# Kernel optimization log

Hardware: AMD Instinct MI355X
Metric: run time of the kernel (lower is better)

The kernel has to match this reference:

```python
import jax, jax.numpy as jnp
import numpy as np

jax.config.update("jax_enable_x64", True)

N_USERS = 100000
N_ITEMS = 50000
N = N_USERS + N_ITEMS          # total nodes
E = 4_000_000                  # nnz of adj
MASK_DEPTH = 2
KEEP_RATE = 0.1
N_SEEDS = 500


def setup_inputs() -> dict:
    key = jax.random.key(0)
    k1, k2, k3, k4 = jax.random.split(key, 4)
    rows = jax.random.randint(k1, (E,), 0, N, dtype=jnp.int64)
    cols = jax.random.randint(k2, (E,), 0, N, dtype=jnp.int64)
    seeds = jax.random.randint(k3, (N_SEEDS,), 0, N, dtype=jnp.int64)
    adj_vals = jax.random.uniform(k4, (E,), dtype=jnp.float32)
    return {"adj_vals": adj_vals, "rows": rows, "cols": cols, "seeds": seeds}


def _mask_subgraphs(adj_vals, rows, cols, seeds, key):
    # --- vectorized BFS-style edge masking (equivalent to the serial per-seed
    # loop: the set of removed edges per depth is the union over the frontier,
    # and collected endpoints are identical to the sequential version) ---
    alive = jnp.ones(E, dtype=bool)                    # edges not yet masked
    frontier = jnp.zeros(N, dtype=bool).at[seeds].set(True)
    masked_nodes = frontier                            # maskNodes accumulator
    for i in range(MASK_DEPTH):
        idct = (frontier[rows] | frontier[cols]) & alive
        alive = alive & ~idct
        if i != MASK_DEPTH - 1:
            hits = (jnp.zeros(N, jnp.int32)
                    .at[rows].add(idct.astype(jnp.int32))
                    .at[cols].add(idct.astype(jnp.int32)))
            frontier = hits > 0                        # unique(concat(nxtSeeds))
            masked_nodes = masked_nodes | frontier
    # random augmentation of the masked node set
    samp_num = int(N * KEEP_RATE)
    ks, kr, kc = jax.random.split(key, 3)
    sampled = jax.random.randint(ks, (samp_num,), 0, N)
    masked_nodes = masked_nodes.at[sampled].set(True)

    # --- encoderAdj: remaining edges with value 1, symmetric degree norm ---
    alive_f = alive.astype(jnp.float32)
    deg = jnp.zeros(N, jnp.float32).at[rows].add(alive_f)   # sparse row sum
    dnorm = jnp.power(deg + 1e-12, -0.5)
    enc_vals = alive_f * dnorm[rows] * dnorm[cols]          # 0 for masked edges

    # --- decoderAdj: random edges among masked nodes + self loops + remaining
    # edges, dedup'd through the row*N+col hash ---
    order = jnp.argsort(~masked_nodes)        # masked node ids first, ascending
    tem_num = masked_nodes.sum()
    i1 = jnp.minimum((jax.random.uniform(kr, (E,)) * tem_num).astype(jnp.int64),
                     tem_num - 1)
    i2 = jnp.minimum((jax.random.uniform(kc, (E,)) * tem_num).astype(jnp.int64),
                     tem_num - 1)
    tr = order[i1]
    tc = order[i2]
    ar = jnp.arange(N, dtype=jnp.int64)
    # masked (dead) edges collapse onto the (0,0) self-loop hash so the
    # fixed-size unique removes them, mirroring the compaction in torch
    h_tail = jnp.where(alive, rows * N + cols, 0)
    hashv = jnp.concatenate([tr * N + tc, tc * N + tr, ar * (N + 1), h_tail])
    uniq = jnp.unique(hashv, size=hashv.shape[0], fill_value=-1)
    valid = uniq >= 0
    dec_vals = valid.astype(jnp.float32)
    dec_cols = jnp.where(valid, uniq % N, 0)
    dec_rows = jnp.where(valid, uniq // N, 0)
    return rows, cols, enc_vals, dec_rows, dec_cols, dec_vals


def reference(adj_vals, rows, cols, seeds):
    key = jax.random.key(42)
    # returns (encoder indices+values, decoder indices+values); padded decoder
    # slots carry value 0 (equivalent sparse matrix)
    return _mask_subgraphs(adj_vals, rows, cols, seeds, key)
```

## Files before the change

kernel.cpp:

```cpp
#include <hip/hip_runtime.h>
#include <stdint.h>

#define NNODE   150000
#define NNODE16 150016
#define EDGES   4000000
#define NSEED   500
#define NSAMP   15000
#define MOUT    12150000
#define SENTK   0xFFFFFFFFFFFFFFFFULL
#define SPAN    150000ULL
#define MULTK   51616ULL
#define FIXED   8150000


#define CHUNK   8192
#define TH      512
#define NC      1488
#define NCX     (NC / 8)
#define MP      ((size_t)NC * CHUNK)
#define RADIX   512
#define NHIST   (RADIX * NC)
#define SNT     (NHIST / 4096)
#define NTILE   NC

#define EBLK    2048
#define ENB     ((EDGES + EBLK - 1) / EBLK)

#define VNB     ((EDGES + 1023) / 1024)

#define MTILE   2048
#define MB      ((NNODE + MTILE - 1) / MTILE)

#define OUT_DR  12000000
#define OUT_DC  24150000
#define OUT_DV  36300000

__host__ __device__ inline void tf2x32(uint32_t k0, uint32_t k1,
                                       uint32_t x0, uint32_t x1,
                                       uint32_t& o0, uint32_t& o1) {
  uint32_t ks2 = k0 ^ k1 ^ 0x1BD11BDAu;
  x0 += k0; x1 += k1;
#define TFR(d) { x0 += x1; x1 = (x1 << d) | (x1 >> (32 - d)); x1 ^= x0; }
  TFR(13) TFR(15) TFR(26) TFR(6)
  x0 += k1; x1 += ks2 + 1u;
  TFR(17) TFR(29) TFR(16) TFR(24)
  x0 += ks2; x1 += k0 + 2u;
  TFR(13) TFR(15) TFR(26) TFR(6)
  x0 += k0; x1 += k1 + 3u;
  TFR(17) TFR(29) TFR(16) TFR(24)
  x0 += k1; x1 += ks2 + 4u;
  TFR(13) TFR(15) TFR(26) TFR(6)
  x0 += ks2; x1 += k0 + 5u;
#undef TFR
  o0 = x0; o1 = x1;
}

__device__ inline unsigned long long tf_bits64(uint32_t k0, uint32_t k1, uint32_t i) {
  uint32_t o0, o1;
  tf2x32(k0, k1, 0u, i, o0, o1);
  return ((unsigned long long)o0 << 32) | o1;
}

__device__ inline int activeChunks(const int* counters) {
  int m2 = FIXED + counters[2];
  return (m2 + CHUNK - 1) / CHUNK;
}

__device__ inline int block_excl_scan_256(int v, int* lds , int& total) {
  int lane = threadIdx.x & 63, wid = threadIdx.x >> 6;
  int inc = v;
#pragma unroll
  for (int off = 1; off < 64; off <<= 1) {
    int y = __shfl_up(inc, off, 64);
    if (lane >= off) inc += y;
  }
  if (lane == 63) lds[wid] = inc;
  __syncthreads();
  if (threadIdx.x == 0) {
    int a = 0;
#pragma unroll
    for (int w = 0; w < 4; ++w) { int t = lds[w]; lds[w] = a; a += t; }
    lds[4] = a;
  }
  __syncthreads();
  total = lds[4];
  int res = inc - v + lds[wid];
  __syncthreads();
  return res;
}

__device__ inline void scan512_x4(const int v[4], int ex[4], int tot[4], int* aux) {
  int lane = threadIdx.x & 63, wid = threadIdx.x >> 6;
  int inc[4];
#pragma unroll
  for (int j = 0; j < 4; ++j) inc[j] = v[j];
#pragma unroll
  for (int off = 1; off < 64; off <<= 1) {
#pragma unroll
    for (int j = 0; j < 4; ++j) {
      int y = __shfl_up(inc[j], off, 64);
      if (lane >= off) inc[j] += y;
    }
  }
  if (lane == 63) {
#pragma unroll
    for (int j = 0; j < 4; ++j) aux[j * 8 + wid] = inc[j];
  }
  __syncthreads();
  if (threadIdx.x == 0) {
#pragma unroll
    for (int j = 0; j < 4; ++j) {
      int a = 0;
#pragma unroll
      for (int w = 0; w < 8; ++w) { int t = aux[j * 8 + w]; aux[j * 8 + w] = a; a += t; }
      aux[32 + j] = a;
    }
  }
  __syncthreads();
#pragma unroll
  for (int j = 0; j < 4; ++j) {
    ex[j] = inc[j] - v[j] + aux[j * 8 + wid];
    tot[j] = aux[32 + j];
  }
}

__device__ inline int scan512_1(int v, int* aux ) {
  int lane = threadIdx.x & 63, wid = threadIdx.x >> 6;
  int inc = v;
#pragma unroll
  for (int off = 1; off < 64; off <<= 1) {
    int y = __shfl_up(inc, off, 64);
    if (lane >= off) inc += y;
  }
  if (lane == 63) aux[wid] = inc;
  __syncthreads();
  if (threadIdx.x == 0) {
    int a = 0;
#pragma unroll
    for (int w = 0; w < 8; ++w) { int t = aux[w]; aux[w] = a; a += t; }
  }
  __syncthreads();
  return inc - v + aux[wid];
}

__device__ inline int lookback64(volatile unsigned*, unsigned* state, int tile) {
  int lane = threadIdx.x;
  int acc = 0, cur = tile;
  for (;;) {
    int idx = cur - 1 - lane;
    unsigned v = 0;
    if (idx >= 0) {
      v = __hip_atomic_load(&state[idx], __ATOMIC_ACQUIRE, __HIP_MEMORY_SCOPE_AGENT);
      while ((v >> 30) == 0u)
        v = __hip_atomic_load(&state[idx], __ATOMIC_ACQUIRE, __HIP_MEMORY_SCOPE_AGENT);
    }
    unsigned st = (idx >= 0) ? (v >> 30) : 0u;
    int val = (int)(v & 0x3FFFFFFFu);
    unsigned long long pm = __ballot(st == 2u);
    int stop = pm ? (__ffsll((unsigned long long)pm) - 1) : 64;
    int contrib = (idx >= 0 && lane <= stop) ? val : 0;
#pragma unroll
    for (int off = 32; off; off >>= 1) contrib += __shfl_down(contrib, off, 64);
    acc += __shfl(contrib, 0, 64);
    if (stop < 64) break;
    cur -= 64;
  }
  return acc;
}

__device__ inline int phys16(int p) { return (p & ~15) | ((p + (p >> 4)) & 15); }

__global__ __launch_bounds__(256) void k_seed(const int* seeds, uint8_t* frontier, uint8_t* masked) {
  int i = blockIdx.x * 256 + threadIdx.x;
  if (i < NSEED) { int v = seeds[i]; frontier[v] = 1; masked[v] = 1; }
}

__global__ __launch_bounds__(256) void k_bfs0(const int* rows, const int* cols,
                                              const uint8_t* frontier, uint8_t* alive, uint8_t* nxt,
                                              float* out) {
  int g = blockIdx.x * 1024 + threadIdx.x * 4;
  if (g >= EDGES) return;
  if (g + 4 <= EDGES) {
    int4 r4 = *(const int4*)&rows[g];
    int4 c4 = *(const int4*)&cols[g];
    int rr[4] = {r4.x, r4.y, r4.z, r4.w};
    int cc[4] = {c4.x, c4.y, c4.z, c4.w};
    *(float4*)&out[g] = make_float4((float)rr[0], (float)rr[1], (float)rr[2], (float)rr[3]);
    *(float4*)&out[EDGES + g] = make_float4((float)cc[0], (float)cc[1], (float)cc[2], (float)cc[3]);
    uint8_t al[4];
#pragma unroll
    for (int k = 0; k < 4; ++k) {
      int hit = frontier[rr[k]] | frontier[cc[k]];
      al[k] = (uint8_t)(1 - hit);
      if (hit) { nxt[rr[k]] = 1; nxt[cc[k]] = 1; }
    }
    *(uchar4*)&alive[g] = make_uchar4(al[0], al[1], al[2], al[3]);
  } else {
    for (int e = g; e < EDGES; ++e) {
      int r = rows[e], c = cols[e];
      out[e] = (float)r;
      out[EDGES + e] = (float)c;
      int hit = frontier[r] | frontier[c];
      alive[e] = (uint8_t)(1 - hit);
      if (hit) { nxt[r] = 1; nxt[c] = 1; }
    }
  }
}

__global__ __launch_bounds__(256) void k_bfs1deg(const int* rows, const int* cols,
                                                 const uint8_t* nxt, uint8_t* alive, int* deg8) {
  int g = blockIdx.x * 1024 + threadIdx.x * 4;
  if (g >= EDGES) return;
  int* dmy = deg8 + (blockIdx.x & 7) * NNODE16;
  if (g + 4 <= EDGES) {
    int4 r4 = *(const int4*)&rows[g];
    int4 c4 = *(const int4*)&cols[g];
    uchar4 a4 = *(const uchar4*)&alive[g];
    int rr[4] = {r4.x, r4.y, r4.z, r4.w};
    int cc[4] = {c4.x, c4.y, c4.z, c4.w};
    uint8_t aa[4] = {a4.x, a4.y, a4.z, a4.w};
    uint8_t na[4];
#pragma unroll
    for (int k = 0; k < 4; ++k) {
      int a = aa[k];
      if (a && (nxt[rr[k]] | nxt[cc[k]])) a = 0;
      na[k] = (uint8_t)a;
    }
    *(uchar4*)&alive[g] = make_uchar4(na[0], na[1], na[2], na[3]);
#pragma unroll
    for (int k = 0; k < 4; ++k)
      if (na[k]) atomicAdd(&dmy[rr[k]], 1);
  } else {
    for (int e = g; e < EDGES; ++e) {
      int a = alive[e];
      int r = rows[e];
      if (a && (nxt[r] | nxt[cols[e]])) { alive[e] = 0; a = 0; }
      if (a) atomicAdd(&dmy[r], 1);
    }
  }
}

__global__ __launch_bounds__(256) void k_sample(uint8_t* masked,
                                                uint32_t a0, uint32_t a1, uint32_t b0, uint32_t b1) {
  int i = blockIdx.x * 256 + threadIdx.x;
  if (i >= NSAMP) return;
  unsigned long long hi = tf_bits64(a0, a1, (uint32_t)i);
  unsigned long long lo = tf_bits64(b0, b1, (uint32_t)i);
  unsigned long long off = ((hi % SPAN) * MULTK + (lo % SPAN)) % SPAN;
  masked[off] = 1;
}

__global__ __launch_bounds__(256) void k_dnorm(const int* deg8, float* dnorm,
                                               uint8_t* masked, const uint8_t* nxt) {
  int v = blockIdx.x * 256 + threadIdx.x;
  if (v < NNODE) {
    int s = 0;
#pragma unroll
    for (int j = 0; j < 8; ++j) s += deg8[j * NNODE16 + v];
    float x = (float)s + 1e-12f;
    dnorm[v] = (float)(1.0 / sqrt((double)x));
    masked[v] |= nxt[v];
  }
}

__global__ __launch_bounds__(256) void k_enctail(const int* rows, const int* cols,
                                                 const uint8_t* alive, const float* dnorm,
                                                 float* out, unsigned long long* A, int* counters) {
  __shared__ int lds[8];
  __shared__ unsigned long long stage[EBLK];
  __shared__ int sbase;
  int base = blockIdx.x * EBLK;
  unsigned long long vv[8];
  int emit[8], c = 0;
#pragma unroll
  for (int k = 0; k < 8; ++k) {
    int e = base + k * 256 + threadIdx.x;
    emit[k] = 0;
    if (e < EDGES) {
      int r = rows[e], cc = cols[e];
      int a = alive[e];
      out[2 * EDGES + e] = a ? dnorm[r] * dnorm[cc] : 0.0f;
      unsigned long long v = ((unsigned long long)(unsigned)r << 18) | (unsigned)cc;
      if (a && v) { emit[k] = 1; vv[k] = v; c++; }
    }
  }
  int total;
  int ex = block_excl_scan_256(c, lds, total);
#pragma unroll
  for (int k = 0; k < 8; ++k) {
    if (emit[k]) stage[ex++] = vv[k];
  }
  if (threadIdx.x == 0) sbase = total ? atomicAdd(&counters[2], total) : 0;
  __syncthreads();
  int sb = sbase;
  for (int i = threadIdx.x; i < total; i += 256)
    A[(size_t)FIXED + sb + i] = stage[i];
}

__global__ __launch_bounds__(256) void k_mreduce(const uint8_t* masked, int* mPart) {
  __shared__ int lds[4];
  int base = blockIdx.x * MTILE;
  int s = 0;
  for (int i = threadIdx.x; i < MTILE; i += 256) {
    int idx = base + i;
    if (idx < NNODE) s += masked[idx];
  }
#pragma unroll
  for (int off = 32; off; off >>= 1) s += __shfl_down(s, off, 64);
  if ((threadIdx.x & 63) == 0) lds[threadIdx.x >> 6] = s;
  __syncthreads();
  if (threadIdx.x == 0) mPart[blockIdx.x] = lds[0] + lds[1] + lds[2] + lds[3];
}

__global__ __launch_bounds__(1024) void k_scan_small(int* part, int m, int* totalOut) {
  __shared__ int a[2048];
  int tid = threadIdx.x;
  a[tid] = (tid < m) ? part[tid] : 0;
  a[tid + 1024] = (tid + 1024 < m) ? part[tid + 1024] : 0;
  __syncthreads();
  for (int off = 1; off < 2048; off <<= 1) {
    int v1 = 0, v2;
    if (tid >= off) v1 = a[tid - off];
    v2 = a[tid + 1024 - off];
    __syncthreads();
    if (tid >= off) a[tid] += v1;
    a[tid + 1024] += v2;
    __syncthreads();
  }
  if (tid < m) part[tid] = (tid == 0) ? 0 : a[tid - 1];
  if (tid + 1024 < m) part[tid + 1024] = a[tid + 1023];
  if (tid == 0 && totalOut) *totalOut = a[2047];
}

__global__ __launch_bounds__(256) void k_mscatter(const uint8_t* masked, const int* mPart, int* mlist) {
  __shared__ int lds[8];
  int t0 = blockIdx.x * MTILE + threadIdx.x * 8;
  int c = 0;
#pragma unroll
  for (int k = 0; k < 8; ++k) { int idx = t0 + k; c += (idx < NNODE) ? masked[idx] : 0; }
  int total;
  int ex = block_excl_scan_256(c, lds, total);
  int run = mPart[blockIdx.x] + ex;
#pragma unroll
  for (int k = 0; k < 8; ++k) {
    int idx = t0 + k;
    if (idx < NNODE && masked[idx]) mlist[run++] = idx;
  }
}

__global__ __launch_bounds__(256) void k_build_pairs(const int* mlist, const int* counters,
                                                     unsigned long long* A,
                                                     uint32_t r0, uint32_t r1, uint32_t c0, uint32_t c1) {
  int e = blockIdx.x * 256 + threadIdx.x;
  long long tem = counters[1];
  unsigned long long bits = tf_bits64(r0, r1, (uint32_t)e);
  double u1 = __longlong_as_double((long long)((bits >> 12) | 0x3FF0000000000000ULL)) - 1.0;
  long long i1 = (long long)(u1 * (double)tem); if (i1 > tem - 1) i1 = tem - 1;
  bits = tf_bits64(c0, c1, (uint32_t)e);
  double u2 = __longlong_as_double((long long)((bits >> 12) | 0x3FF0000000000000ULL)) - 1.0;
  long long i2 = (long long)(u2 * (double)tem); if (i2 > tem - 1) i2 = tem - 1;
  unsigned long long tr = (unsigned long long)mlist[i1];
  unsigned long long tc = (unsigned long long)mlist[i2];
  A[2 * (size_t)e]     = (tr << 18) | tc;
  A[2 * (size_t)e + 1] = (tc << 18) | tr;
}

__global__ __launch_bounds__(256) void k_build_self(unsigned long long* A) {
  int v = blockIdx.x * 256 + threadIdx.x;
  if (v >= NNODE) return;
  unsigned long long u = (unsigned long long)v;
  A[2 * (size_t)EDGES + v] = (u << 18) | u;
}

__global__ __launch_bounds__(256) void k_pad(unsigned long long* A, const int* counters) {
  int m2 = FIXED + counters[2];
  int ac = (m2 + CHUNK - 1) / CHUNK;
  size_t idx = (size_t)m2 + blockIdx.x * 256 + threadIdx.x;
  if (idx < (size_t)ac * CHUNK) A[idx] = SENTK;
}

__global__ __launch_bounds__(TH) void k_rhist2(const unsigned long long* __restrict__ src,
                                               int* __restrict__ hist, int shift,
                                               const int* counters) {
  __shared__ int h8[RADIX * 4];
  int tid = threadIdx.x;
  int ac = activeChunks(counters);
  if ((int)blockIdx.x >= ac) { hist[(size_t)tid * NC + blockIdx.x] = 0; return; }
  for (int i = tid; i < RADIX * 4; i += TH) h8[i] = 0;
  __syncthreads();
  const ulonglong2* s2 = (const ulonglong2*)(src + (size_t)blockIdx.x * CHUNK);
  int rep = tid & 3, scnt = 0;
#pragma unroll
  for (int r = 0; r < 8; ++r) {
    ulonglong2 v = s2[tid + r * TH];
    int d0 = (int)((v.x >> shift) & (RADIX - 1));
    int d1 = (int)((v.y >> shift) & (RADIX - 1));
    if (d0 == RADIX - 1) scnt++; else atomicAdd(&h8[d0 * 4 + rep], 1);
    if (d1 == RADIX - 1) scnt++; else atomicAdd(&h8[d1 * 4 + rep], 1);
  }
  if (scnt) atomicAdd(&h8[(RADIX - 1) * 4 + rep], scnt);
  __syncthreads();
  int4 hv = *(const int4*)&h8[tid * 4];
  hist[(size_t)tid * NC + blockIdx.x] = hv.x + hv.y + hv.z + hv.w;
}

__global__ __launch_bounds__(256) void k_scan_lb(int* __restrict__ g,
                                                 unsigned* __restrict__ tstate) {
  __shared__ int lds[8];
  __shared__ int sbase;
  int tile = blockIdx.x;
  int base = tile * 4096 + threadIdx.x * 16;
  int x[16];
  {
    int4 q0 = *(const int4*)&g[base];
    int4 q1 = *(const int4*)&g[base + 4];
    int4 q2 = *(const int4*)&g[base + 8];
    int4 q3 = *(const int4*)&g[base + 12];
    x[0]=q0.x; x[1]=q0.y; x[2]=q0.z;  x[3]=q0.w;
    x[4]=q1.x; x[5]=q1.y; x[6]=q1.z;  x[7]=q1.w;
    x[8]=q2.x; x[9]=q2.y; x[10]=q2.z; x[11]=q2.w;
    x[12]=q3.x; x[13]=q3.y; x[14]=q3.z; x[15]=q3.w;
  }
  int s = 0;
#pragma unroll
  for (int k = 0; k < 16; ++k) { int t = x[k]; x[k] = s; s += t; }
  int total;
  int ex = block_excl_scan_256(s, lds, total);
  if (threadIdx.x == 0) {
    unsigned st = (tile == 0) ? 0x80000000u : 0x40000000u;
    __hip_atomic_store(&tstate[tile], st | (unsigned)total,
                       __ATOMIC_RELEASE, __HIP_MEMORY_SCOPE_AGENT);
    if (tile == 0) sbase = 0;
  }
  if (tile > 0 && threadIdx.x < 64) {
    int acc = lookback64(nullptr, tstate, tile);
    if (threadIdx.x == 0) {
      sbase = acc;
      __hip_atomic_store(&tstate[tile], 0x80000000u | (unsigned)(acc + total),
                         __ATOMIC_RELEASE, __HIP_MEMORY_SCOPE_AGENT);
    }
  }
  __syncthreads();
  int bb = sbase + ex;
#pragma unroll
  for (int k = 0; k < 16; ++k) x[k] += bb;
  *(int4*)&g[base]      = make_int4(x[0], x[1], x[2], x[3]);
  *(int4*)&g[base + 4]  = make_int4(x[4], x[5], x[6], x[7]);
  *(int4*)&g[base + 8]  = make_int4(x[8], x[9], x[10], x[11]);
  *(int4*)&g[base + 12] = make_int4(x[12], x[13], x[14], x[15]);
}

__global__ __launch_bounds__(TH) void k_rscatter2(const unsigned long long* __restrict__ src,
                                                  unsigned long long* __restrict__ dst,
                                                  const int* __restrict__ hist, int shift,
                                                  const int* counters) {
  __shared__ unsigned long long kk[CHUNK];
  __shared__ int h8[RADIX * 4];
  __shared__ int dstart[RADIX], gbase[RADIX];
  __shared__ int aux[40];
  int tid = threadIdx.x;
  int chunk = (blockIdx.x & 7) * NCX + (blockIdx.x >> 3);
  int ac = activeChunks(counters);
  if (chunk >= ac) return;
  size_t cbase = (size_t)chunk * CHUNK;
  gbase[tid] = hist[(size_t)tid * NC + chunk];
  for (int i = tid; i < RADIX * 4; i += TH) h8[i] = 0;
  __syncthreads();
  int rep = tid & 3;
  const ulonglong2* s2 = (const ulonglong2*)(src + cbase);
  int scnt = 0;
#pragma unroll
  for (int r = 0; r < 8; ++r) {
    ulonglong2 v = s2[tid + r * TH];
    int i = 2 * (tid + r * TH);
    kk[phys16(i)] = v.x;
    kk[phys16(i + 1)] = v.y;
    int d0 = (int)((v.x >> shift) & (RADIX - 1));
    int d1 = (int)((v.y >> shift) & (RADIX - 1));
    if (d0 == RADIX - 1) scnt++; else atomicAdd(&h8[d0 * 4 + rep], 1);
    if (d1 == RADIX - 1) scnt++; else atomicAdd(&h8[d1 * 4 + rep], 1);
  }
  if (scnt) atomicAdd(&h8[(RADIX - 1) * 4 + rep], scnt);
  __syncthreads();
  int4 hv = *(const int4*)&h8[tid * 4];
  int h = hv.x + hv.y + hv.z + hv.w;
  int ex0 = scan512_1(h, aux);
  dstart[tid] = ex0;
  __syncthreads();
  int t0 = tid * 16;
  for (int rr = 0; rr < 3; ++rr) {
    int sh = shift + 3 * rr;
    unsigned long long key[16];
    unsigned long long cpack = 0;
#pragma unroll
    for (int k = 0; k < 16; ++k) {
      key[k] = kk[phys16(t0 + k)];
      cpack += 1ULL << (((int)(key[k] >> sh) & 7) << 3);
    }
    int v4[4], ex[4], tot[4];
#pragma unroll
    for (int j = 0; j < 4; ++j) {
      unsigned pair = (unsigned)(cpack >> (16 * j));
      v4[j] = (int)((pair & 0xffu) | ((pair & 0xff00u) << 8));
    }
    scan512_x4(v4, ex, tot, aux);
    unsigned long long startq0, startq1;
    {
      int a = 0, s8[8];
#pragma unroll
      for (int j = 0; j < 4; ++j) {
        int tlo = tot[j] & 0xffff, thi = tot[j] >> 16;
        int elo = ex[j] & 0xffff,  ehi = ex[j] >> 16;
        s8[2 * j]     = a + elo; a += tlo;
        s8[2 * j + 1] = a + ehi; a += thi;
      }
      startq0 = (unsigned long long)(unsigned)s8[0]
              | ((unsigned long long)(unsigned)s8[1] << 16)
              | ((unsigned long long)(unsigned)s8[2] << 32)
              | ((unsigned long long)(unsigned)s8[3] << 48);
      startq1 = (unsigned long long)(unsigned)s8[4]
              | ((unsigned long long)(unsigned)s8[5] << 16)
              | ((unsigned long long)(unsigned)s8[6] << 32)
              | ((unsigned long long)(unsigned)s8[7] << 48);
    }
#pragma unroll
    for (int k = 0; k < 16; ++k) {
      int d = (int)(key[k] >> sh) & 7;
      int fs = (d & 3) << 4;
      unsigned long long inc = 1ULL << fs;
      int pos;
      if (d < 4) { pos = (int)((startq0 >> fs) & 0xffffu); startq0 += inc; }
      else       { pos = (int)((startq1 >> fs) & 0xffffu); startq1 += inc; }
      kk[phys16(pos)] = key[k];
    }
    __syncthreads();
  }
#pragma unroll
  for (int r = 0; r < 16; ++r) {
    int i = tid + r * TH;
    unsigned long long k1 = kk[phys16(i)];
    int d = (int)((k1 >> shift) & (RADIX - 1));
    dst[(size_t)(gbase[d] + (i - dstart[d]))] = k1;
  }
}

__global__ __launch_bounds__(TH) void k_final_lb(const unsigned long long* __restrict__ A,
                                                 unsigned* __restrict__ ustate,
                                                 int* __restrict__ counters,
                                                 float* __restrict__ out) {
  __shared__ int aux[9];
  __shared__ float sq[CHUNK], sr[CHUNK];
  __shared__ int scnt, stile, sbase;
  if (threadIdx.x == 0) stile = atomicAdd(&counters[4], 1);
  int ac = activeChunks(counters);
  __syncthreads();
  int tile = stile;
  if (tile >= ac) return;
  size_t base = (size_t)tile * CHUNK + (size_t)threadIdx.x * 16;
  unsigned long long v[16];
  int f[16], c = 0;
  unsigned long long prev = (base == 0) ? 0ULL : A[base - 1];
#pragma unroll
  for (int k = 0; k < 16; ++k) {
    v[k] = A[base + k];
    f[k] = (v[k] != SENTK && v[k] != prev) ? 1 : 0;
    c += f[k];
    prev = v[k];
  }
  int ex = scan512_1(c, aux);
  if (threadIdx.x == TH - 1) scnt = ex + c;
  __syncthreads();
  int cnt = scnt;
  if (threadIdx.x == 0) {
    unsigned st = (tile == 0) ? 0x80000000u : 0x40000000u;
    __hip_atomic_store(&ustate[tile], st | (unsigned)cnt,
                       __ATOMIC_RELEASE, __HIP_MEMORY_SCOPE_AGENT);
    if (tile == 0) sbase = 0;
  }
  if (tile > 0 && threadIdx.x < 64) {
    int acc = lookback64(nullptr, ustate, tile);
    if (threadIdx.x == 0) {
      sbase = acc;
      __hip_atomic_store(&ustate[tile], 0x80000000u | (unsigned)(acc + cnt),
                         __ATOMIC_RELEASE, __HIP_MEMORY_SCOPE_AGENT);
    }
  }
  int j = ex;
#pragma unroll
  for (int k = 0; k < 16; ++k) {
    if (f[k]) {
      unsigned long long val = v[k];
      sq[j] = (float)(long long)(val >> 18);
      sr[j] = (float)(long long)(val & 262143ULL);
      j++;
    }
  }
  __syncthreads();
  if (threadIdx.x == 0 && tile == ac - 1) counters[3] = sbase + cnt;
  int jb = 1 + sbase;
  for (int i = (int)threadIdx.x; i < cnt; i += TH) {
    out[OUT_DR + jb + i] = sq[i];
    out[OUT_DC + jb + i] = sr[i];
  }
}

__global__ __launch_bounds__(256) void k_dectail(const int* counters, float* out) {
  int i = (blockIdx.x * 256 + threadIdx.x) * 4;
  if (i >= MOUT) return;
  int totU = counters[3] + 1;
  float4 dv;
  dv.x = (i + 0 < totU) ? 1.0f : 0.0f;
  dv.y = (i + 1 < totU) ? 1.0f : 0.0f;
  dv.z = (i + 2 < totU) ? 1.0f : 0.0f;
  dv.w = (i + 3 < totU) ? 1.0f : 0.0f;
  *(float4*)&out[OUT_DV + i] = dv;
  if (i + 3 >= totU) {
    float4 z = make_float4(0.0f, 0.0f, 0.0f, 0.0f);
    if (i >= totU) {
      *(float4*)&out[OUT_DR + i] = z;
      *(float4*)&out[OUT_DC + i] = z;
    } else {
#pragma unroll
      for (int k = 0; k < 4; ++k)
        if (i + k >= totU) { out[OUT_DR + i + k] = 0.0f; out[OUT_DC + i + k] = 0.0f; }
    }
  }
  if (i == 0) { out[OUT_DR] = 0.0f; out[OUT_DC] = 0.0f; }
}

extern "C" void kernel_launch(void* const* d_in, const int* in_sizes, int n_in,
                              void* d_out, int out_size, void* d_ws, size_t ws_size,
                              hipStream_t stream) {
  const int* rows = (const int*)d_in[1];
  const int* cols = (const int*)d_in[2];
  const int* seeds = (const int*)d_in[3];
  float* out = (float*)d_out;

  char* ws = (char*)d_ws;
  size_t off = 0;
  auto alloc = [&](size_t bytes) -> char* {
    char* p = ws + off;
    off += (bytes + 255) & ~(size_t)255;
    return p;
  };
  unsigned long long* A = (unsigned long long*)alloc(MP * 8);
  uint8_t* alive = (uint8_t*)alloc(EDGES);
  char* zbase = ws + off;
  uint8_t* frontier = (uint8_t*)alloc(NNODE);
  uint8_t* nextf = (uint8_t*)alloc(NNODE);
  uint8_t* masked = (uint8_t*)alloc(NNODE);
  int* deg8 = (int*)alloc((size_t)8 * NNODE16 * 4);
  int* counters = (int*)alloc(256 * 4);
  unsigned* tstate = (unsigned*)alloc((size_t)4 * 256 * 4);
  unsigned* ustate = (unsigned*)alloc((size_t)NTILE * 4);
  size_t zsize = (size_t)((ws + off) - zbase);
  float* dnorm = (float*)alloc((size_t)NNODE * 4);
  int* mlist = (int*)alloc((size_t)NNODE * 4);
  int* hist = (int*)alloc((size_t)NHIST * 4);
  int* mPart = (int*)alloc(256 * 4);

  unsigned long long* Bbuf = (unsigned long long*)(out + OUT_DR);

  uint32_t ks0, ks1, kr0, kr1, kc0, kc1, s10, s11, s20, s21;
  tf2x32(0u, 42u, 0u, 0u, ks0, ks1);
  tf2x32(0u, 42u, 0u, 1u, kr0, kr1);
  tf2x32(0u, 42u, 0u, 2u, kc0, kc1);
  tf2x32(ks0, ks1, 0u, 0u, s10, s11);
  tf2x32(ks0, ks1, 0u, 1u, s20, s21);

  hipMemsetAsync(zbase, 0, zsize, stream);

  const int EB = EDGES / 256;
  const int NB = (NNODE + 255) / 256;

  k_seed<<<2, 256, 0, stream>>>(seeds, frontier, masked);
  k_bfs0<<<VNB, 256, 0, stream>>>(rows, cols, frontier, alive, nextf, out);
  k_bfs1deg<<<VNB, 256, 0, stream>>>(rows, cols, nextf, alive, deg8);
  k_sample<<<(NSAMP + 255) / 256, 256, 0, stream>>>(masked, s10, s11, s20, s21);
  k_dnorm<<<NB, 256, 0, stream>>>(deg8, dnorm, masked, nextf);
  k_enctail<<<ENB, 256, 0, stream>>>(rows, cols, alive, dnorm, out, A, counters);

  k_mreduce<<<MB, 256, 0, stream>>>(masked, mPart);
  k_scan_small<<<1, 1024, 0, stream>>>(mPart, MB, counters + 1);
  k_mscatter<<<MB, 256, 0, stream>>>(masked, mPart, mlist);

  k_build_pairs<<<EB, 256, 0, stream>>>(mlist, counters, A, kr0, kr1, kc0, kc1);
  k_build_self<<<NB, 256, 0, stream>>>(A);
  k_pad<<<CHUNK / 256, 256, 0, stream>>>(A, counters);

  unsigned long long* src = A;
  unsigned long long* dst = Bbuf;
  const int shifts[4] = {0, 9, 18, 27};
  for (int p = 0; p < 4; ++p) {
    k_rhist2<<<NC, TH, 0, stream>>>(src, hist, shifts[p], counters);
    k_scan_lb<<<SNT, 256, 0, stream>>>(hist, tstate + (size_t)p * 256);
    k_rscatter2<<<NC, TH, 0, stream>>>(src, dst, hist, shifts[p], counters);
    unsigned long long* t = src; src = dst; dst = t;
  }

  k_final_lb<<<NTILE, TH, 0, stream>>>(src, ustate, counters, out);
  k_dectail<<<(MOUT / 4 + 255) / 256, 256, 0, stream>>>(counters, out);
}
```

Before: 1.105 ms.

## Replace decoupled-lookback unique compaction with count, scan, scatter passes

The final dedup compaction used a single-pass decoupled lookback across tiles with an atomic tile counter. It is replaced by three kernels: a per-chunk unique count, a small scan of the partial counts, and a scatter that stages the chunk in LDS with vectorized loads before writing. This removes the serial inter-block lookback chain, but the sorted array is now read twice and two extra launches are added.

```diff
diff --git a/kernel.cpp b/kernel.cpp
--- a/kernel.cpp
+++ b/kernel.cpp
@@ -143,7 +143,7 @@
   return inc - v + aux[wid];
 }
 
-__device__ inline int lookback64(volatile unsigned*, unsigned* state, int tile) {
+__device__ inline int lookback64(unsigned* state, int tile) {
   int lane = threadIdx.x;
   int acc = 0, cur = tile;
   for (;;) {
@@ -433,7 +433,7 @@
     if (tile == 0) sbase = 0;
   }
   if (tile > 0 && threadIdx.x < 64) {
-    int acc = lookback64(nullptr, tstate, tile);
+    int acc = lookback64(tstate, tile);
     if (threadIdx.x == 0) {
       sbase = acc;
       __hip_atomic_store(&tstate[tile], 0x80000000u | (unsigned)(acc + total),
@@ -544,61 +544,88 @@
   }
 }
 
-__global__ __launch_bounds__(TH) void k_final_lb(const unsigned long long* __restrict__ A,
-                                                 unsigned* __restrict__ ustate,
-                                                 int* __restrict__ counters,
-                                                 float* __restrict__ out) {
+__global__ __launch_bounds__(TH) void k_uniq_count(const unsigned long long* __restrict__ A,
+                                                   int* __restrict__ uPart,
+                                                   const int* counters) {
+  __shared__ int lds[8];
+  int ac = activeChunks(counters);
+  if ((int)blockIdx.x >= ac) { if (threadIdx.x == 0) uPart[blockIdx.x] = 0; return; }
+  int tid = threadIdx.x;
+  int lane = tid & 63, w = tid >> 6;
+  size_t wbase = (size_t)blockIdx.x * CHUNK + (size_t)w * 1024;
+  unsigned long long carry = (wbase == 0) ? 0ULL : A[wbase - 1];
+  int c = 0;
+#pragma unroll
+  for (int r = 0; r < 8; ++r) {
+    ulonglong2 v = *(const ulonglong2*)&A[wbase + r * 128 + lane * 2];
+    unsigned long long pl = __shfl_up(v.y, 1, 64);
+    unsigned long long last = __shfl(v.y, 63, 64);
+    unsigned long long p0 = (lane == 0) ? carry : pl;
+    c += (v.x != SENTK && v.x != p0) ? 1 : 0;
+    c += (v.y != SENTK && v.y != v.x) ? 1 : 0;
+    carry = last;
+  }
+#pragma unroll
+  for (int off = 32; off; off >>= 1) c += __shfl_down(c, off, 64);
+  if (lane == 0) lds[w] = c;
+  __syncthreads();
+  if (tid == 0) {
+    int s = 0;
+#pragma unroll
+    for (int q = 0; q < 8; ++q) s += lds[q];
+    uPart[blockIdx.x] = s;
+  }
+}
+
+__global__ __launch_bounds__(TH) void k_final(const unsigned long long* __restrict__ A,
+                                              const int* __restrict__ uPart,
+                                              const int* counters, float* __restrict__ out) {
+  __shared__ unsigned long long kk[CHUNK];
   __shared__ int aux[9];
-  __shared__ float sq[CHUNK], sr[CHUNK];
-  __shared__ int scnt, stile, sbase;
-  if (threadIdx.x == 0) stile = atomicAdd(&counters[4], 1);
+  __shared__ int sscnt;
   int ac = activeChunks(counters);
-  __syncthreads();
-  int tile = stile;
-  if (tile >= ac) return;
-  size_t base = (size_t)tile * CHUNK + (size_t)threadIdx.x * 16;
+  if ((int)blockIdx.x >= ac) return;
+  int tid = threadIdx.x;
+  size_t cb = (size_t)blockIdx.x * CHUNK;
+  const ulonglong2* s2 = (const ulonglong2*)(A + cb);
+#pragma unroll
+  for (int r = 0; r < 8; ++r) {
+    ulonglong2 v = s2[tid + r * TH];
+    int i = 2 * (tid + r * TH);
+    kk[phys16(i)] = v.x;
+    kk[phys16(i + 1)] = v.y;
+  }
+  __syncthreads();
+  int t0 = tid * 16;
   unsigned long long v[16];
   int f[16], c = 0;
-  unsigned long long prev = (base == 0) ? 0ULL : A[base - 1];
+  unsigned long long prev = (t0 == 0) ? ((cb == 0) ? 0ULL : A[cb - 1])
+                                      : kk[phys16(t0 - 1)];
 #pragma unroll
   for (int k = 0; k < 16; ++k) {
-    v[k] = A[base + k];
+    v[k] = kk[phys16(t0 + k)];
     f[k] = (v[k] != SENTK && v[k] != prev) ? 1 : 0;
     c += f[k];
     prev = v[k];
   }
   int ex = scan512_1(c, aux);
-  if (threadIdx.x == TH - 1) scnt = ex + c;
-  __syncthreads();
-  int cnt = scnt;
-  if (threadIdx.x == 0) {
-    unsigned st = (tile == 0) ? 0x80000000u : 0x40000000u;
-    __hip_atomic_store(&ustate[tile], st | (unsigned)cnt,
-                       __ATOMIC_RELEASE, __HIP_MEMORY_SCOPE_AGENT);
-    if (tile == 0) sbase = 0;
-  }
-  if (tile > 0 && threadIdx.x < 64) {
-    int acc = lookback64(nullptr, ustate, tile);
-    if (threadIdx.x == 0) {
-      sbase = acc;
-      __hip_atomic_store(&ustate[tile], 0x80000000u | (unsigned)(acc + cnt),
-                         __ATOMIC_RELEASE, __HIP_MEMORY_SCOPE_AGENT);
-    }
-  }
+  if (tid == TH - 1) sscnt = ex + c;
+  __syncthreads();
+  float* sq = (float*)kk;
+  float* sr = sq + CHUNK;
   int j = ex;
 #pragma unroll
   for (int k = 0; k < 16; ++k) {
     if (f[k]) {
-      unsigned long long val = v[k];
-      sq[j] = (float)(long long)(val >> 18);
-      sr[j] = (float)(long long)(val & 262143ULL);
+      sq[j] = (float)(unsigned)(v[k] >> 18);
+      sr[j] = (float)(unsigned)(v[k] & 262143u);
       j++;
     }
   }
   __syncthreads();
-  if (threadIdx.x == 0 && tile == ac - 1) counters[3] = sbase + cnt;
-  int jb = 1 + sbase;
-  for (int i = (int)threadIdx.x; i < cnt; i += TH) {
+  int cnt = sscnt;
+  int jb = 1 + uPart[blockIdx.x];
+  for (int i = tid; i < cnt; i += TH) {
     out[OUT_DR + jb + i] = sq[i];
     out[OUT_DC + jb + i] = sr[i];
   }
@@ -652,11 +679,11 @@
   int* deg8 = (int*)alloc((size_t)8 * NNODE16 * 4);
   int* counters = (int*)alloc(256 * 4);
   unsigned* tstate = (unsigned*)alloc((size_t)4 * 256 * 4);
-  unsigned* ustate = (unsigned*)alloc((size_t)NTILE * 4);
   size_t zsize = (size_t)((ws + off) - zbase);
   float* dnorm = (float*)alloc((size_t)NNODE * 4);
   int* mlist = (int*)alloc((size_t)NNODE * 4);
   int* hist = (int*)alloc((size_t)NHIST * 4);
+  int* uPart = (int*)alloc(2048 * 4);
   int* mPart = (int*)alloc(256 * 4);
 
   unsigned long long* Bbuf = (unsigned long long*)(out + OUT_DR);
@@ -698,6 +725,8 @@
     unsigned long long* t = src; src = dst; dst = t;
   }
 
-  k_final_lb<<<NTILE, TH, 0, stream>>>(src, ustate, counters, out);
+  k_uniq_count<<<NTILE, TH, 0, stream>>>(src, uPart, counters);
+  k_scan_small<<<1, 1024, 0, stream>>>(uPart, NTILE, counters + 3);
+  k_final<<<NTILE, TH, 0, stream>>>(src, uPart, counters, out);
   k_dectail<<<(MOUT / 4 + 255) / 256, 256, 0, stream>>>(counters, out);
 }
```

Result: faster. 992.6 us (-10.2%).
